# Kernel optimization log

Hardware: AMD Instinct MI355X
Metric: run time of the kernel (lower is better)

## Reference

```python
import jax, jax.numpy as jnp
import numpy as np

NUM_NODES = 100000
NUM_EDGES = 500000
HID = 256


def setup_inputs() -> dict:
    key = jax.random.key(0)
    ks = jax.random.split(key, 6)
    emb_src = jax.random.normal(ks[0], (NUM_NODES, HID), dtype=jnp.float32)
    emb_dst = jax.random.normal(ks[1], (NUM_NODES, HID), dtype=jnp.float32)
    edge_label_index = jax.random.randint(ks[2], (2, NUM_EDGES), 0, NUM_NODES, dtype=jnp.int32)
    # torch Linear(2H, H) weight is [H, 2H]; we store transposed [2H, H] for x @ W
    W1 = jax.random.normal(ks[3], (2 * HID, HID), dtype=jnp.float32) * (1.0 / np.sqrt(2 * HID))
    b1 = jnp.zeros((HID,), dtype=jnp.float32)
    W2 = jax.random.normal(ks[4], (HID, 1), dtype=jnp.float32) * (1.0 / np.sqrt(HID))
    b2 = jnp.zeros((1,), dtype=jnp.float32)
    return {"emb_src": emb_src, "emb_dst": emb_dst, "edge_label_index": edge_label_index,
            "W1": W1, "b1": b1, "W2": W2, "b2": b2}


def reference(emb_src, emb_dst, edge_label_index, W1, b1, W2, b2):
    # decode(): gather src/dst embeddings, concat, Linear-ReLU-Linear, squeeze
    src_idx = edge_label_index[0]
    dst_idx = edge_label_index[1]
    h_src = emb_src[src_idx]          # [E, H] irregular gather
    h_dst = emb_dst[dst_idx]          # [E, H]
    # concat([h_src, h_dst]) @ W1 == h_src @ W1[:H] + h_dst @ W1[H:]
    # (avoids materializing the [E, 2H] concatenated tensor)
    h = jnp.dot(h_src, W1[:HID]) + jnp.dot(h_dst, W1[HID:]) + b1  # [E, H]
    h = jax.nn.relu(h)
    logits = (jnp.dot(h, W2) + b2)[:, 0]  # [E]
    return logits
```

## Files before the change

### kernel.cpp

```cpp
#include <hip/hip_runtime.h>
#include <hip/hip_bf16.h>
#include <stdint.h>

#define HID 256
#define BM  64
#define LDA 68
#define LDC 264

typedef __bf16 bf16x8 __attribute__((ext_vector_type(8)));
typedef float  f32x4  __attribute__((ext_vector_type(4)));

__device__ __forceinline__ ushort f2bf(float x) {
    union { float f; uint32_t u; } v; v.f = x;
    uint32_t u = v.u;
    uint32_t r = u + 0x7fffu + ((u >> 16) & 1u);
    return (ushort)(r >> 16);
}

__device__ __forceinline__ uint32_t pack2bf(float a, float b) {
    union { float f; uint32_t u; } ua, ub;
    ua.f = a; ub.f = b;
    return __builtin_amdgcn_perm(ub.u + 0x8000u, ua.u + 0x8000u, 0x07060302u);
}

__device__ __forceinline__ float uaf(uint32_t x) {
    union { uint32_t u; float f; } c; c.u = x; return c.f;
}

__global__ void conv_w1(const float* __restrict__ W1, ushort* __restrict__ Wt3) {
    __shared__ ushort tr[32][33];
    const int bk = blockIdx.x >> 3;
    const int bn = blockIdx.x & 7;
    const int t  = threadIdx.x;
    #pragma unroll
    for (int i = 0; i < 4; ++i) {
        int e = t + 256 * i; int r = e >> 5, cc = e & 31;
        tr[cc][r] = f2bf(W1[(size_t)(bk * 32 + r) * HID + bn * 32 + cc]);
    }
    __syncthreads();
    #pragma unroll
    for (int i = 0; i < 4; ++i) {
        int e = t + 256 * i; int rn = e >> 5, ck = e & 31;
        int k = bk * 32 + ck; int c = k >> 6; int kk = k & 63;
        Wt3[((size_t)c * HID + bn * 32 + rn) * 64 + kk] = tr[rn][ck];
    }
}

__global__ __launch_bounds__(256, 3)
void node_gemm(const float* __restrict__ emb0, const float* __restrict__ emb1,
               const ushort* __restrict__ Wt3,
               ushort* __restrict__ u0, ushort* __restrict__ u1,
               int n0, int n1, int nb0) {
    __shared__ union {
        ushort As[2][BM * LDA];
        ushort Cs[BM * LDC];
    } sm;

    const int t    = threadIdx.x;
    const int tb   = (blockIdx.x >= nb0) ? 1 : 0;
    const int bloc = blockIdx.x - tb * nb0;
    const float*  emb = tb ? emb1 : emb0;
    ushort*       uo  = tb ? u1 : u0;
    const int     n   = tb ? n1 : n0;
    const int     e0  = bloc * BM;

    const int wave = t >> 6, lane = t & 63, q = lane >> 4, cl = lane & 15;

    const int rr = t >> 2, ss = (t & 3) * 16;
    int grow = e0 + rr; if (grow > n - 1) grow = n - 1;
    const float* abase = emb + (size_t)grow * HID + ss;

    float4 g[4];
    auto gather = [&](int c) {
        const float4* p = reinterpret_cast<const float4*>(abase + c * 64);
        #pragma unroll
        for (int i = 0; i < 4; ++i) g[i] = p[i];
    };
    auto cvstore = [&](int buf) {
        uint4 v0, v1;
        v0.x = pack2bf(g[0].x, g[0].y); v0.y = pack2bf(g[0].z, g[0].w);
        v0.z = pack2bf(g[1].x, g[1].y); v0.w = pack2bf(g[1].z, g[1].w);
        v1.x = pack2bf(g[2].x, g[2].y); v1.y = pack2bf(g[2].z, g[2].w);
        v1.z = pack2bf(g[3].x, g[3].y); v1.w = pack2bf(g[3].z, g[3].w);
        *reinterpret_cast<uint4*>(&sm.As[buf][rr * LDA + ss])     = v0;
        *reinterpret_cast<uint4*>(&sm.As[buf][rr * LDA + ss + 8]) = v1;
    };

    gather(0); cvstore(0);
    __syncthreads();

    f32x4 acc[4][4] = {};

    #pragma unroll
    for (int c = 0; c < 4; ++c) {
        const int cur = c & 1;
        if (c < 3) gather(c + 1);
        #pragma unroll
        for (int ks = 0; ks < 2; ++ks) {
            bf16x8 af[4], bfr[4];
            #pragma unroll
            for (int mi = 0; mi < 4; ++mi)
                af[mi] = *reinterpret_cast<const bf16x8*>(
                    &sm.As[cur][(mi * 16 + cl) * LDA + ks * 32 + q * 8]);
            const int cg = tb * 4 + c;
            #pragma unroll
            for (int ni = 0; ni < 4; ++ni)
                bfr[ni] = *reinterpret_cast<const bf16x8*>(
                    Wt3 + ((size_t)cg * HID + wave * 64 + ni * 16 + cl) * 64 + ks * 32 + q * 8);
            #pragma unroll
            for (int mi = 0; mi < 4; ++mi)
                #pragma unroll
                for (int ni = 0; ni < 4; ++ni)
                    acc[mi][ni] = __builtin_amdgcn_mfma_f32_16x16x32_bf16(
                        af[mi], bfr[ni], acc[mi][ni], 0, 0, 0);
        }
        if (c < 3) { cvstore(cur ^ 1); __syncthreads(); }
    }

    __syncthreads();
    #pragma unroll
    for (int mi = 0; mi < 4; ++mi)
        #pragma unroll
        for (int ni = 0; ni < 4; ++ni)
            #pragma unroll
            for (int r = 0; r < 4; ++r)
                sm.Cs[(mi * 16 + q * 4 + r) * LDC + wave * 64 + ni * 16 + cl] =
                    f2bf(acc[mi][ni][r]);
    __syncthreads();

    const int srow = t >> 2, scol = (t & 3) * 64;
    if (e0 + srow < n) {
        ushort* dst = uo + (size_t)(e0 + srow) * HID + scol;
        #pragma unroll
        for (int i = 0; i < 8; ++i) {
            uint4 w = *reinterpret_cast<const uint4*>(&sm.Cs[srow * LDC + scol + i * 8]);
            *reinterpret_cast<uint4*>(dst + i * 8) = w;
        }
    }
}

__global__ __launch_bounds__(256, 4)
void lp_edge(const ushort* __restrict__ u, const ushort* __restrict__ v,
             const int* __restrict__ eli,
             const float* __restrict__ b1, const float* __restrict__ W2,
             const float* __restrict__ b2, float* __restrict__ out,
             int E, int nwaves) {
    const int lane = threadIdx.x & 63;
    const int half = lane >> 5, sub = lane & 31;
    const int wid  = blockIdx.x * (blockDim.x >> 6) + (threadIdx.x >> 6);

    float b1v[8], w2v[8];
    {
        const float4* p1 = reinterpret_cast<const float4*>(b1 + sub * 8);
        const float4* p2 = reinterpret_cast<const float4*>(W2 + sub * 8);
        float4 a = p1[0], b = p1[1], c = p2[0], d = p2[1];
        b1v[0]=a.x; b1v[1]=a.y; b1v[2]=a.z; b1v[3]=a.w;
        b1v[4]=b.x; b1v[5]=b.y; b1v[6]=b.z; b1v[7]=b.w;
        w2v[0]=c.x; w2v[1]=c.y; w2v[2]=c.z; w2v[3]=c.w;
        w2v[4]=d.x; w2v[5]=d.y; w2v[6]=d.z; w2v[7]=d.w;
    }
    const float bias2 = b2[0];
    const ushort* tab  = half ? v : u;
    const int*    idxp = eli + (size_t)half * E;

    for (int base = wid * 8; base < E; base += nwaves * 8) {
        uint4 g[8];
        #pragma unroll
        for (int j = 0; j < 8; ++j) {
            int e = base + j; if (e > E - 1) e = E - 1;
            int row = idxp[e];
            g[j] = *reinterpret_cast<const uint4*>(tab + (size_t)row * HID + sub * 8);
        }
        float res = 0.f;
        #pragma unroll
        for (int j = 0; j < 8; ++j) {
            uint32_t pd[4], gd[4] = { g[j].x, g[j].y, g[j].z, g[j].w };
            #pragma unroll
            for (int c = 0; c < 4; ++c) pd[c] = (uint32_t)__shfl_xor((int)gd[c], 32);
            float acc = 0.f;
            #pragma unroll
            for (int c = 0; c < 4; ++c) {
                float a0 = uaf(gd[c] << 16), a1 = uaf(gd[c] & 0xffff0000u);
                float o0 = uaf(pd[c] << 16), o1 = uaf(pd[c] & 0xffff0000u);
                float h0 = fmaxf(a0 + o0 + b1v[2 * c], 0.f);
                float h1 = fmaxf(a1 + o1 + b1v[2 * c + 1], 0.f);
                acc = fmaf(h0, w2v[2 * c], acc);
                acc = fmaf(h1, w2v[2 * c + 1], acc);
            }
            #pragma unroll
            for (int m = 1; m <= 16; m <<= 1) acc += __shfl_xor(acc, m);
            if (half == 0 && sub == j) res = acc + bias2;
        }
        int e = base + sub;
        if (half == 0 && sub < 8 && e < E) out[e] = res;
    }
}

template<int USEWT>
__global__ __launch_bounds__(256, 3)
void lp_mono(const float* __restrict__ es, const float* __restrict__ ed,
             const int* __restrict__ eli,
             const ushort* __restrict__ Wt3, const float* __restrict__ W1,
             const float* __restrict__ b1, const float* __restrict__ W2,
             const float* __restrict__ b2,
             float* __restrict__ out, int E) {
    __shared__ __align__(16) ushort As[2][BM * LDA];
    __shared__ int   sIdx[2][BM];
    __shared__ float hred[4][BM];

    const int t = threadIdx.x, e0 = blockIdx.x * BM;
    const int wave = t >> 6, lane = t & 63, q = lane >> 4, cl = lane & 15;

    if (t < 2 * BM) {
        int which = t >> 6, e = t & 63;
        int ge = e0 + e; if (ge > E - 1) ge = E - 1;
        sIdx[which][e] = eli[which * E + ge];
    }
    __syncthreads();

    int ge_[2], go_[2], rsrc[2], rdst[2];
    #pragma unroll
    for (int i = 0; i < 2; ++i) {
        int c2 = t + 256 * i;
        ge_[i] = c2 >> 3; go_[i] = c2 & 7;
        rsrc[i] = sIdx[0][ge_[i]];
        rdst[i] = sIdx[1][ge_[i]];
    }
    float4 g0[2], g1[2];
    auto gather = [&](int c) {
        const float* tab = (c < 4) ? es : ed;
        #pragma unroll
        for (int i = 0; i < 2; ++i) {
            int row = (c < 4) ? rsrc[i] : rdst[i];
            const float* p = tab + (size_t)row * HID + (c & 3) * 64 + go_[i] * 8;
            g0[i] = *reinterpret_cast<const float4*>(p);
            g1[i] = *reinterpret_cast<const float4*>(p + 4);
        }
    };
    auto cvstore = [&](int buf) {
        #pragma unroll
        for (int i = 0; i < 2; ++i) {
            uint4 v;
            v.x = pack2bf(g0[i].x, g0[i].y); v.y = pack2bf(g0[i].z, g0[i].w);
            v.z = pack2bf(g1[i].x, g1[i].y); v.w = pack2bf(g1[i].z, g1[i].w);
            *reinterpret_cast<uint4*>(&As[buf][ge_[i] * LDA + go_[i] * 8]) = v;
        }
    };
    gather(0); cvstore(0); __syncthreads();
    f32x4 acc[4][4] = {};
    #pragma unroll
    for (int c = 0; c < 8; ++c) {
        const int cur = c & 1;
        if (c < 7) gather(c + 1);
        #pragma unroll
        for (int ks = 0; ks < 2; ++ks) {
            bf16x8 af[4], bfr[4];
            #pragma unroll
            for (int mi = 0; mi < 4; ++mi)
                af[mi] = *reinterpret_cast<const bf16x8*>(
                    &As[cur][(mi * 16 + cl) * LDA + ks * 32 + q * 8]);
            #pragma unroll
            for (int ni = 0; ni < 4; ++ni) {
                int n = wave * 64 + ni * 16 + cl;
                if (USEWT) {
                    bfr[ni] = *reinterpret_cast<const bf16x8*>(
                        Wt3 + ((size_t)c * HID + n) * 64 + ks * 32 + q * 8);
                } else {
                    union { ushort s[8]; bf16x8 v; } u;
                    #pragma unroll
                    for (int j = 0; j < 8; ++j)
                        u.s[j] = f2bf(W1[(size_t)(c * 64 + ks * 32 + q * 8 + j) * HID + n]);
                    bfr[ni] = u.v;
                }
            }
            #pragma unroll
            for (int mi = 0; mi < 4; ++mi)
                #pragma unroll
                for (int ni = 0; ni < 4; ++ni)
                    acc[mi][ni] = __builtin_amdgcn_mfma_f32_16x16x32_bf16(
                        af[mi], bfr[ni], acc[mi][ni], 0, 0, 0);
        }
        if (c < 7) { cvstore(cur ^ 1); __syncthreads(); }
    }
    float b1v[4], w2v[4];
    #pragma unroll
    for (int ni = 0; ni < 4; ++ni) {
        int col = wave * 64 + ni * 16 + cl;
        b1v[ni] = b1[col]; w2v[ni] = W2[col];
    }
    #pragma unroll
    for (int mi = 0; mi < 4; ++mi) {
        #pragma unroll
        for (int r = 0; r < 4; ++r) {
            float s = 0.f;
            #pragma unroll
            for (int ni = 0; ni < 4; ++ni) {
                float h = acc[mi][ni][r] + b1v[ni];
                h = fmaxf(h, 0.f);
                s += h * w2v[ni];
            }
            s += __shfl_xor(s, 1); s += __shfl_xor(s, 2);
            s += __shfl_xor(s, 4); s += __shfl_xor(s, 8);
            if (cl == 0) hred[wave][mi * 16 + q * 4 + r] = s;
        }
    }
    __syncthreads();
    if (t < BM) {
        int ge = e0 + t;
        if (ge < E)
            out[ge] = hred[0][t] + hred[1][t] + hred[2][t] + hred[3][t] + b2[0];
    }
}

extern "C" void kernel_launch(void* const* d_in, const int* in_sizes, int n_in,
                              void* d_out, int out_size, void* d_ws, size_t ws_size,
                              hipStream_t stream) {
    const float* emb_src = (const float*)d_in[0];
    const float* emb_dst = (const float*)d_in[1];
    const int*   eli     = (const int*)d_in[2];
    const float* W1      = (const float*)d_in[3];
    const float* b1      = (const float*)d_in[4];
    const float* W2      = (const float*)d_in[5];
    const float* b2      = (const float*)d_in[6];
    float*       out     = (float*)d_out;

    const int E   = in_sizes[2] / 2;
    const int n0n = in_sizes[0] / HID;
    const int n1n = in_sizes[1] / HID;

    const size_t wtB = (size_t)8 * HID * 64 * sizeof(ushort);
    const size_t uB  = (size_t)n0n * HID * sizeof(ushort);
    const size_t vB  = (size_t)n1n * HID * sizeof(ushort);

    ushort* Wt3 = (ushort*)d_ws;
    ushort* u0  = (ushort*)((char*)d_ws + wtB);
    ushort* u1  = (ushort*)((char*)d_ws + wtB + uB);

    const int haveWt   = ws_size >= wtB;
    const int fullPath = ws_size >= wtB + uB + vB;

    if (haveWt)
        conv_w1<<<128, 256, 0, stream>>>(W1, Wt3);

    if (fullPath) {
        const int nb0 = (n0n + BM - 1) / BM;
        const int nb1 = (n1n + BM - 1) / BM;
        node_gemm<<<nb0 + nb1, 256, 0, stream>>>(emb_src, emb_dst, Wt3,
                                                 u0, u1, n0n, n1n, nb0);
        const int eb = 1024;
        lp_edge<<<eb, 256, 0, stream>>>(u0, u1, eli, b1, W2, b2, out, E, eb * 4);
    } else if (haveWt) {
        const int nb = (E + BM - 1) / BM;
        lp_mono<1><<<nb, 256, 0, stream>>>(emb_src, emb_dst, eli, Wt3, W1,
                                           b1, W2, b2, out, E);
    } else {
        const int nb = (E + BM - 1) / BM;
        lp_mono<0><<<nb, 256, 0, stream>>>(emb_src, emb_dst, eli, Wt3, W1,
                                           b1, W2, b2, out, E);
    }
}
```

Before: 362.3 us.

## Load node-GEMM A operands directly into MFMA registers, drop LDS staging

Node GEMM now reads fp32 embedding rows straight from global memory into registers in MFMA fragment order, converts them to bf16 in-register, and skips the double-buffered LDS tile and its barriers. W1 is repacked into a k-group-of-8 layout so each B fragment is one contiguous 16-byte load. The edge kernel's occupancy hint rises from 4 to 8 and its grid doubles to 2048 blocks, and the Wt-only fallback path is removed. The cost is uncoalesced global reads, since each lane fetches 32-byte pieces from 16 different rows, and more registers live in the node GEMM.

Result: slower. 392.9 us (+8.4%).

```diff
diff --git a/kernel.cpp b/kernel.cpp
--- a/kernel.cpp
+++ b/kernel.cpp
@@ -27,7 +27,7 @@
     union { uint32_t u; float f; } c; c.u = x; return c.f;
 }
 
-__global__ void conv_w1(const float* __restrict__ W1, ushort* __restrict__ Wt3) {
+__global__ void conv_w1(const float* __restrict__ W1, ushort* __restrict__ Wt4) {
     __shared__ ushort tr[32][33];
     const int bk = blockIdx.x >> 3;
     const int bn = blockIdx.x & 7;
@@ -41,20 +41,20 @@
     #pragma unroll
     for (int i = 0; i < 4; ++i) {
         int e = t + 256 * i; int rn = e >> 5, ck = e & 31;
-        int k = bk * 32 + ck; int c = k >> 6; int kk = k & 63;
-        Wt3[((size_t)c * HID + bn * 32 + rn) * 64 + kk] = tr[rn][ck];
+        int k = bk * 32 + ck;
+        int grp = k >> 3;
+        int j   = k & 7;
+        int n   = bn * 32 + rn;
+        Wt4[((size_t)grp * HID + n) * 8 + j] = tr[rn][ck];
     }
 }
 
 __global__ __launch_bounds__(256, 3)
 void node_gemm(const float* __restrict__ emb0, const float* __restrict__ emb1,
-               const ushort* __restrict__ Wt3,
+               const ushort* __restrict__ Wt4,
                ushort* __restrict__ u0, ushort* __restrict__ u1,
                int n0, int n1, int nb0) {
-    __shared__ union {
-        ushort As[2][BM * LDA];
-        ushort Cs[BM * LDC];
-    } sm;
+    __shared__ ushort Cs[BM * LDC];
 
     const int t    = threadIdx.x;
     const int tb   = (blockIdx.x >= nb0) ? 1 : 0;
@@ -66,65 +66,57 @@
 
     const int wave = t >> 6, lane = t & 63, q = lane >> 4, cl = lane & 15;
 
-    const int rr = t >> 2, ss = (t & 3) * 16;
-    int grow = e0 + rr; if (grow > n - 1) grow = n - 1;
-    const float* abase = emb + (size_t)grow * HID + ss;
-
-    float4 g[4];
-    auto gather = [&](int c) {
-        const float4* p = reinterpret_cast<const float4*>(abase + c * 64);
-        #pragma unroll
-        for (int i = 0; i < 4; ++i) g[i] = p[i];
-    };
-    auto cvstore = [&](int buf) {
-        uint4 v0, v1;
-        v0.x = pack2bf(g[0].x, g[0].y); v0.y = pack2bf(g[0].z, g[0].w);
-        v0.z = pack2bf(g[1].x, g[1].y); v0.w = pack2bf(g[1].z, g[1].w);
-        v1.x = pack2bf(g[2].x, g[2].y); v1.y = pack2bf(g[2].z, g[2].w);
-        v1.z = pack2bf(g[3].x, g[3].y); v1.w = pack2bf(g[3].z, g[3].w);
-        *reinterpret_cast<uint4*>(&sm.As[buf][rr * LDA + ss])     = v0;
-        *reinterpret_cast<uint4*>(&sm.As[buf][rr * LDA + ss + 8]) = v1;
-    };
-
-    gather(0); cvstore(0);
-    __syncthreads();
+    const float* arow[4];
+    #pragma unroll
+    for (int mi = 0; mi < 4; ++mi) {
+        int r = e0 + mi * 16 + cl; if (r > n - 1) r = n - 1;
+        arow[mi] = emb + (size_t)r * HID + q * 8;
+    }
+    const ushort* bb = Wt4 + ((size_t)q * HID + wave * 64 + cl) * 8;
 
     f32x4 acc[4][4] = {};
 
     #pragma unroll
     for (int c = 0; c < 4; ++c) {
-        const int cur = c & 1;
-        if (c < 3) gather(c + 1);
-        #pragma unroll
-        for (int ks = 0; ks < 2; ++ks) {
-            bf16x8 af[4], bfr[4];
-            #pragma unroll
-            for (int mi = 0; mi < 4; ++mi)
-                af[mi] = *reinterpret_cast<const bf16x8*>(
-                    &sm.As[cur][(mi * 16 + cl) * LDA + ks * 32 + q * 8]);
-            const int cg = tb * 4 + c;
+        bf16x8 bfr[2][4];
+        #pragma unroll
+        for (int ks = 0; ks < 2; ++ks)
             #pragma unroll
             for (int ni = 0; ni < 4; ++ni)
-                bfr[ni] = *reinterpret_cast<const bf16x8*>(
-                    Wt3 + ((size_t)cg * HID + wave * 64 + ni * 16 + cl) * 64 + ks * 32 + q * 8);
-            #pragma unroll
-            for (int mi = 0; mi < 4; ++mi)
+                bfr[ks][ni] = *reinterpret_cast<const bf16x8*>(
+                    bb + (((size_t)((tb * 4 + c) * 2 + ks) * 4) * HID + ni * 16) * 8);
+        float4 a0[2][4], a1[2][4];
+        #pragma unroll
+        for (int ks = 0; ks < 2; ++ks)
+            #pragma unroll
+            for (int mi = 0; mi < 4; ++mi) {
+                const float* p = arow[mi] + c * 64 + ks * 32;
+                a0[ks][mi] = *reinterpret_cast<const float4*>(p);
+                a1[ks][mi] = *reinterpret_cast<const float4*>(p + 4);
+            }
+        #pragma unroll
+        for (int ks = 0; ks < 2; ++ks)
+            #pragma unroll
+            for (int mi = 0; mi < 4; ++mi) {
+                union { uint32_t d[4]; bf16x8 v; } af;
+                af.d[0] = pack2bf(a0[ks][mi].x, a0[ks][mi].y);
+                af.d[1] = pack2bf(a0[ks][mi].z, a0[ks][mi].w);
+                af.d[2] = pack2bf(a1[ks][mi].x, a1[ks][mi].y);
+                af.d[3] = pack2bf(a1[ks][mi].z, a1[ks][mi].w);
                 #pragma unroll
                 for (int ni = 0; ni < 4; ++ni)
                     acc[mi][ni] = __builtin_amdgcn_mfma_f32_16x16x32_bf16(
-                        af[mi], bfr[ni], acc[mi][ni], 0, 0, 0);
-        }
-        if (c < 3) { cvstore(cur ^ 1); __syncthreads(); }
-    }
-
-    __syncthreads();
+                        af.v, bfr[ks][ni], acc[mi][ni], 0, 0, 0);
+            }
+    }
+
     #pragma unroll
     for (int mi = 0; mi < 4; ++mi)
         #pragma unroll
         for (int ni = 0; ni < 4; ++ni)
             #pragma unroll
             for (int r = 0; r < 4; ++r)
-                sm.Cs[(mi * 16 + q * 4 + r) * LDC + wave * 64 + ni * 16 + cl] =
+                Cs[(mi * 16 + q * 4 + r) * LDC + wave * 64 + ni * 16 + cl] =
                     f2bf(acc[mi][ni][r]);
     __syncthreads();
 
@@ -133,13 +125,13 @@
         ushort* dst = uo + (size_t)(e0 + srow) * HID + scol;
         #pragma unroll
         for (int i = 0; i < 8; ++i) {
-            uint4 w = *reinterpret_cast<const uint4*>(&sm.Cs[srow * LDC + scol + i * 8]);
+            uint4 w = *reinterpret_cast<const uint4*>(&Cs[srow * LDC + scol + i * 8]);
             *reinterpret_cast<uint4*>(dst + i * 8) = w;
         }
     }
 }
 
-__global__ __launch_bounds__(256, 4)
+__global__ __launch_bounds__(256, 8)
 void lp_edge(const ushort* __restrict__ u, const ushort* __restrict__ v,
              const int* __restrict__ eli,
              const float* __restrict__ b1, const float* __restrict__ W2,
@@ -196,11 +188,9 @@
     }
 }
 
-template<int USEWT>
 __global__ __launch_bounds__(256, 3)
 void lp_mono(const float* __restrict__ es, const float* __restrict__ ed,
-             const int* __restrict__ eli,
-             const ushort* __restrict__ Wt3, const float* __restrict__ W1,
+             const int* __restrict__ eli, const float* __restrict__ W1,
              const float* __restrict__ b1, const float* __restrict__ W2,
              const float* __restrict__ b2,
              float* __restrict__ out, int E) {
@@ -261,17 +251,12 @@
                     &As[cur][(mi * 16 + cl) * LDA + ks * 32 + q * 8]);
             #pragma unroll
             for (int ni = 0; ni < 4; ++ni) {
-                int n = wave * 64 + ni * 16 + cl;
-                if (USEWT) {
-                    bfr[ni] = *reinterpret_cast<const bf16x8*>(
-                        Wt3 + ((size_t)c * HID + n) * 64 + ks * 32 + q * 8);
-                } else {
-                    union { ushort s[8]; bf16x8 v; } u;
-                    #pragma unroll
-                    for (int j = 0; j < 8; ++j)
-                        u.s[j] = f2bf(W1[(size_t)(c * 64 + ks * 32 + q * 8 + j) * HID + n]);
-                    bfr[ni] = u.v;
-                }
+                int nn = wave * 64 + ni * 16 + cl;
+                union { ushort s[8]; bf16x8 v; } u;
+                #pragma unroll
+                for (int j = 0; j < 8; ++j)
+                    u.s[j] = f2bf(W1[(size_t)(c * 64 + ks * 32 + q * 8 + j) * HID + nn]);
+                bfr[ni] = u.v;
             }
             #pragma unroll
             for (int mi = 0; mi < 4; ++mi)
@@ -328,34 +313,27 @@
     const int n0n = in_sizes[0] / HID;
     const int n1n = in_sizes[1] / HID;
 
-    const size_t wtB = (size_t)8 * HID * 64 * sizeof(ushort);
+    const size_t wtB = (size_t)2 * HID * 2 * HID * sizeof(ushort);
     const size_t uB  = (size_t)n0n * HID * sizeof(ushort);
     const size_t vB  = (size_t)n1n * HID * sizeof(ushort);
 
-    ushort* Wt3 = (ushort*)d_ws;
+    ushort* Wt4 = (ushort*)d_ws;
     ushort* u0  = (ushort*)((char*)d_ws + wtB);
     ushort* u1  = (ushort*)((char*)d_ws + wtB + uB);
 
-    const int haveWt   = ws_size >= wtB;
     const int fullPath = ws_size >= wtB + uB + vB;
 
-    if (haveWt)
-        conv_w1<<<128, 256, 0, stream>>>(W1, Wt3);
-
     if (fullPath) {
+        conv_w1<<<128, 256, 0, stream>>>(W1, Wt4);
         const int nb0 = (n0n + BM - 1) / BM;
         const int nb1 = (n1n + BM - 1) / BM;
-        node_gemm<<<nb0 + nb1, 256, 0, stream>>>(emb_src, emb_dst, Wt3,
+        node_gemm<<<nb0 + nb1, 256, 0, stream>>>(emb_src, emb_dst, Wt4,
                                                  u0, u1, n0n, n1n, nb0);
-        const int eb = 1024;
+        const int eb = 2048;
         lp_edge<<<eb, 256, 0, stream>>>(u0, u1, eli, b1, W2, b2, out, E, eb * 4);
-    } else if (haveWt) {
-        const int nb = (E + BM - 1) / BM;
-        lp_mono<1><<<nb, 256, 0, stream>>>(emb_src, emb_dst, eli, Wt3, W1,
-                                           b1, W2, b2, out, E);
     } else {
         const int nb = (E + BM - 1) / BM;
-        lp_mono<0><<<nb, 256, 0, stream>>>(emb_src, emb_dst, eli, Wt3, W1,
-                                           b1, W2, b2, out, E);
-    }
-}
+        lp_mono<<<nb, 256, 0, stream>>>(emb_src, emb_dst, eli, W1,
+                                        b1, W2, b2, out, E);
+    }
+}
```
